# Kernel tuning notes

Hardware: AMD Instinct MI355X
Metric: run time of the kernel (lower is better)

## Reference

```python
import jax, jax.numpy as jnp
import numpy as np

BIG_K = 13
EPS = 1e-5  # torch BatchNorm2d default


def setup_inputs() -> dict:
    key = jax.random.key(0)
    k1, k2, k3, k4 = jax.random.split(key, 4)
    B, C1, C2, H, W_ = 8, 256, 256, 64, 64
    x = jax.random.normal(k1, (B, C1, H, W_), dtype=jnp.float32)
    # scale kernel by fan-in so pre-BN activations are O(1)
    fan_in = C1 * BIG_K * BIG_K
    W = jax.random.normal(k2, (C2, C1, BIG_K, BIG_K), dtype=jnp.float32) / np.sqrt(fan_in)
    gamma = jnp.ones((C2,), dtype=jnp.float32)
    beta = jnp.zeros((C2,), dtype=jnp.float32)
    running_mean = jax.random.normal(k3, (C2,), dtype=jnp.float32) * 0.1
    running_var = jax.random.uniform(k4, (C2,), dtype=jnp.float32, minval=0.5, maxval=1.5)
    return {"x": x, "W": W, "gamma": gamma, "beta": beta,
            "running_mean": running_mean, "running_var": running_var}


def reference(x, W, gamma, beta, running_mean, running_var):
    # Fallback path of ShiftWiseConv: big-kernel conv (no bias) -> BN (inference) -> SiLU
    pad = BIG_K // 2
    y = jax.lax.conv_general_dilated(
        x, W,
        window_strides=(1, 1),
        padding=[(pad, pad), (pad, pad)],
        dimension_numbers=("NCHW", "OIHW", "NCHW"),
    )
    inv = gamma * jax.lax.rsqrt(running_var + EPS)  # [C2]
    y = y * inv[None, :, None, None] + (beta - running_mean * inv)[None, :, None, None]
    return jax.nn.silu(y)
```

## Files before the change

### kernel.cpp

```cpp
#include <hip/hip_runtime.h>
#include <stdint.h>

#define EPS 1e-5f

typedef __attribute__((ext_vector_type(8))) __bf16 bf16x8;
typedef __attribute__((ext_vector_type(16))) float f32x16;

__device__ __forceinline__ int swz4(int r) { return (r ^ (r >> 2)) & 3; }

__device__ __forceinline__ unsigned short f2bf(float f) {
  union { float f; unsigned u; } v; v.f = f;
  unsigned r = v.u + 0x7fffu + ((v.u >> 16) & 1u);
  return (unsigned short)(r >> 16);
}

__device__ __forceinline__ void glds16(const unsigned short* g, unsigned short* l) {
  __builtin_amdgcn_global_load_lds(
      (const __attribute__((address_space(1))) void*)g,
      (__attribute__((address_space(3))) void*)l, 16, 0, 0);
}
__device__ __forceinline__ void glds4(const unsigned short* g, unsigned short* l) {
  __builtin_amdgcn_global_load_lds(
      (const __attribute__((address_space(1))) void*)g,
      (__attribute__((address_space(3))) void*)l, 4, 0, 0);
}

template <int N>
__device__ __forceinline__ void vmwait() {
  asm volatile("s_waitcnt vmcnt(%0)" ::"n"(N) : "memory");
}

__global__ __launch_bounds__(256) void pack_w_kernel(
    const float* __restrict__ W, unsigned short* __restrict__ Wp) {
  const int blk = blockIdx.x;
  const int c2 = blk / 13, kh = blk - c2 * 13;
  const int c1 = threadIdx.x;
  const int c2t = c2 >> 7, m = c2 & 127;
  const int c1c = c1 >> 5, c1i = c1 & 31;
  const float* src = W + (((size_t)(c2 * 256 + c1)) * 13 + kh) * 13;
  const int rowoff = (((c1i >> 3) ^ swz4(m)) << 3) + (c1i & 7);
#pragma unroll
  for (int kw = 0; kw < 13; ++kw) {
    const int ks = (kh * 8 + c1c) * 13 + kw;
    const size_t dst = (((size_t)c2t * 1352 + ks) * 128 + m) * 32 + rowoff;
    Wp[dst] = f2bf(src[kw]);
  }
}

__global__ __launch_bounds__(256) void pack_xt_kernel(
    const float* __restrict__ x, unsigned short* __restrict__ xT) {
  const int blk = blockIdx.x;
  const int rowp = blk % 76;
  const int bc = blk / 76;
  const int c1c = bc & 7, b = bc >> 3;
  const int row = rowp - 6;
  const bool rok = (unsigned)row < 64u;
  unsigned short* dst = xT + (size_t)blk * 2560;
  const float* srcb = x + (size_t)(b * 256 + c1c * 32) * 4096 +
                      (rok ? row * 64 : 0);
#pragma unroll
  for (int e = 0; e < 10; ++e) {
    const int idx = e * 256 + threadIdx.x;
    const int colp = idx >> 5, c1i = idx & 31;
    const int ic = colp - 8;
    const float v = (rok && (unsigned)ic < 64u) ? srcb[(size_t)c1i * 4096 + ic] : 0.f;
    dst[colp * 32 + ((((c1i >> 3) ^ swz4(colp)) << 3)) + (c1i & 7)] = f2bf(v);
  }
}

__global__ __launch_bounds__(256, 2) void conv5_kernel(
    const unsigned short* __restrict__ Wp, const unsigned short* __restrict__ xT,
    const float* __restrict__ gamma, const float* __restrict__ beta,
    const float* __restrict__ mean, const float* __restrict__ var,
    float* __restrict__ out) {
  __shared__ __align__(16) unsigned short Abuf[2][8192];
  __shared__ __align__(16) unsigned short Wbuf[2][5120];
  __shared__ float s_scale[128], s_shift[128];

  const int tid = threadIdx.x;
  const int bid = blockIdx.x;
  const int b = bid & 7;
  const int h0 = ((bid >> 3) & 31) * 2;
  const int c2t = bid >> 8;

  const int wid = tid >> 6, lane = tid & 63;
  const int wr = wid >> 1, wc = wid & 1;
  const int l31 = lane & 31, hi2 = lane >> 5;

  if (tid < 128) {
    const int c2 = c2t * 128 + tid;
    const float inv = gamma[c2] * rsqrtf(var[c2] + EPS);
    s_scale[tid] = inv;
    s_shift[tid] = beta[c2] - mean[c2] * inv;
  }

  int aoff[2][2];
#pragma unroll
  for (int mt = 0; mt < 2; ++mt)
#pragma unroll
    for (int ks = 0; ks < 2; ++ks) {
      const int m = wr * 64 + mt * 32 + l31;
      aoff[mt][ks] = m * 64 + (((ks * 2 + hi2) ^ swz4(m)) << 4);
    }
  int ndh[2], nwl[2];
#pragma unroll
  for (int nt = 0; nt < 2; ++nt) {
    const int n = wc * 64 + nt * 32 + l31;
    ndh[nt] = n >> 6;
    nwl[nt] = n & 63;
  }

  const int tid8 = tid * 8, tid2 = tid * 2;
  const int widA = wid * 512, wid128 = wid * 128;

  const size_t c2base = (size_t)c2t * 1352;
  const int bc8 = b * 8;

  auto wtile = [&](int T) -> const unsigned short* {
    const int kh = T >> 3, c1c = T & 7;
    return xT + (size_t)((bc8 + c1c) * 76 + h0 + kh) * 2560;
  };

  f32x16 acc[2][2];
#pragma unroll
  for (int i = 0; i < 2; ++i)
#pragma unroll
    for (int j = 0; j < 2; ++j)
#pragma unroll
      for (int r = 0; r < 16; ++r) acc[i][j][r] = 0.f;

  {
    const unsigned short* at0 = Wp + (c2base << 12);
    const unsigned short* at1 = Wp + ((c2base + 1) << 12);
    glds16(at0 + tid8, &Abuf[0][0] + widA);
    glds16(at0 + 2048 + tid8, &Abuf[0][2048] + widA);
    glds16(at1 + tid8, &Abuf[0][4096] + widA);
    glds16(at1 + 2048 + tid8, &Abuf[0][6144] + widA);
    const unsigned short* ws = wtile(0);
    glds16(ws + tid8, &Wbuf[0][0] + widA);
    glds16(ws + 2048 + tid8, &Wbuf[0][2048] + widA);
    glds4(ws + 4096 + tid2, &Wbuf[0][4096] + wid128);
    glds4(ws + 4608 + tid2, &Wbuf[0][4608] + wid128);
  }

#define CHALF(AB_, WB_, KW_)                                                  \
  {                                                                           \
    _Pragma("unroll") for (int ks = 0; ks < 2; ++ks) {                        \
      const bf16x8 a0 = *(const bf16x8*)((AB_) + aoff[0][ks]);                \
      const bf16x8 a1 = *(const bf16x8*)((AB_) + aoff[1][ks]);                \
      bf16x8 bfr[2];                                                          \
      _Pragma("unroll") for (int nt = 0; nt < 2; ++nt) {                      \
        const int wcoln = nwl[nt] + (KW_) + 2;                                \
        bfr[nt] = *(const bf16x8*)((WB_) + (ndh[nt] * 80 + wcoln) * 64 +      \
                                   (((ks * 2 + hi2) ^ swz4(wcoln)) << 4));    \
      }                                                                       \
      acc[0][0] = __builtin_amdgcn_mfma_f32_32x32x16_bf16(a0, bfr[0],         \
                                                          acc[0][0], 0, 0, 0);\
      acc[0][1] = __builtin_amdgcn_mfma_f32_32x32x16_bf16(a0, bfr[1],         \
                                                          acc[0][1], 0, 0, 0);\
      acc[1][0] = __builtin_amdgcn_mfma_f32_32x32x16_bf16(a1, bfr[0],         \
                                                          acc[1][0], 0, 0, 0);\
      acc[1][1] = __builtin_amdgcn_mfma_f32_32x32x16_bf16(a1, bfr[1],         \
                                                          acc[1][1], 0, 0, 0);\
    }                                                                         \
  }

#define PHASE(PH, KWA, WBA, KWB, WBB, WRT, WSRCP, WDB)                        \
  {                                                                           \
    {                                                                         \
      int sn0 = S0 + 2 * (PH) + 2;                                            \
      if (sn0 >= 1352) sn0 -= 1352;                                           \
      int sn1 = sn0 + 1;                                                      \
      if (sn1 >= 1352) sn1 -= 1352;                                           \
      const unsigned short* at0 = Wp + ((c2base + (size_t)sn0) << 12);        \
      const unsigned short* at1 = Wp + ((c2base + (size_t)sn1) << 12);        \
      unsigned short* ad = &Abuf[((PH) + 1) & 1][0];                          \
      glds16(at0 + tid8, ad + widA);                                          \
      glds16(at0 + 2048 + tid8, ad + 2048 + widA);                            \
      glds16(at1 + tid8, ad + 4096 + widA);                                   \
      glds16(at1 + 2048 + tid8, ad + 6144 + widA);                            \
    }                                                                         \
    if ((WRT) == 1) glds16((WSRCP) + tid8, &Wbuf[(WDB)][0] + widA);           \
    if ((WRT) == 2)                                                           \
      glds16((WSRCP) + 2048 + tid8, &Wbuf[(WDB)][2048] + widA);               \
    if ((WRT) == 3) {                                                         \
      glds4((WSRCP) + 4096 + tid2, &Wbuf[(WDB)][4096] + wid128);              \
      glds4((WSRCP) + 4608 + tid2, &Wbuf[(WDB)][4608] + wid128);              \
    }                                                                         \
    vmwait<((WRT) == 0 ? 4 : ((WRT) == 3 ? 6 : 5))>();                        \
    __builtin_amdgcn_s_barrier();                                             \
    asm volatile("" ::: "memory");                                            \
    {                                                                         \
      const char* abA = (const char*)&Abuf[(PH) & 1][0];                      \
      const char* abB = abA + 8192;                                           \
      const char* wbA = (const char*)&Wbuf[(WBA)][0];                         \
      const char* wbB = (const char*)&Wbuf[(WBB)][0];                         \
      __builtin_amdgcn_s_setprio(1);                                          \
      CHALF(abA, wbA, KWA)                                                    \
      CHALF(abB, wbB, KWB)                                                    \
      __builtin_amdgcn_s_setprio(0);                                          \
    }                                                                         \
    asm volatile("s_waitcnt lgkmcnt(0)" ::: "memory");                        \
    __builtin_amdgcn_s_barrier();                                             \
  }

  for (int u = 0; u < 26; ++u) {
    const int S0 = u * 52;
    const int Tb = u * 4;
    const unsigned short* wt1 = wtile(Tb + 1);
    const unsigned short* wt2 = wtile(Tb + 2);
    const unsigned short* wt3 = wtile(Tb + 3);
    const unsigned short* wt4 = wtile((Tb + 4 == 104) ? 0 : Tb + 4);
    PHASE(0, 0, 0, 1, 0, 0, wt1, 1)
    PHASE(1, 2, 0, 3, 0, 0, wt1, 1)
    PHASE(2, 4, 0, 5, 0, 0, wt1, 1)
    PHASE(3, 6, 0, 7, 0, 1, wt1, 1)
    PHASE(4, 8, 0, 9, 0, 2, wt1, 1)
    PHASE(5, 10, 0, 11, 0, 3, wt1, 1)
    PHASE(6, 12, 0, 0, 1, 0, wt1, 1)
    PHASE(7, 1, 1, 2, 1, 0, wt2, 0)
    PHASE(8, 3, 1, 4, 1, 0, wt2, 0)
    PHASE(9, 5, 1, 6, 1, 1, wt2, 0)
    PHASE(10, 7, 1, 8, 1, 2, wt2, 0)
    PHASE(11, 9, 1, 10, 1, 3, wt2, 0)
    PHASE(12, 11, 1, 12, 1, 0, wt2, 0)
    PHASE(13, 0, 0, 1, 0, 0, wt3, 1)
    PHASE(14, 2, 0, 3, 0, 0, wt3, 1)
    PHASE(15, 4, 0, 5, 0, 0, wt3, 1)
    PHASE(16, 6, 0, 7, 0, 1, wt3, 1)
    PHASE(17, 8, 0, 9, 0, 2, wt3, 1)
    PHASE(18, 10, 0, 11, 0, 3, wt3, 1)
    PHASE(19, 12, 0, 0, 1, 0, wt3, 1)
    PHASE(20, 1, 1, 2, 1, 0, wt4, 0)
    PHASE(21, 3, 1, 4, 1, 0, wt4, 0)
    PHASE(22, 5, 1, 6, 1, 1, wt4, 0)
    PHASE(23, 7, 1, 8, 1, 2, wt4, 0)
    PHASE(24, 9, 1, 10, 1, 3, wt4, 0)
    PHASE(25, 11, 1, 12, 1, 0, wt4, 0)
  }
#undef PHASE
#undef CHALF

  vmwait<0>();

#pragma unroll
  for (int mt = 0; mt < 2; ++mt) {
#pragma unroll
    for (int nt = 0; nt < 2; ++nt) {
      const int n = wc * 64 + nt * 32 + l31;
      const int hh = h0 + (n >> 6), ww = n & 63;
#pragma unroll
      for (int r = 0; r < 16; ++r) {
        const int mloc = (r & 3) + 8 * (r >> 2) + 4 * hi2;
        const int c2l = wr * 64 + mt * 32 + mloc;
        const float y = acc[mt][nt][r] * s_scale[c2l] + s_shift[c2l];
        out[((size_t)(b * 256 + c2t * 128 + c2l)) * 4096 + hh * 64 + ww] =
            y / (1.f + __expf(-y));
      }
    }
  }
}

__global__ void naive_conv_kernel(
    const float* __restrict__ x, const float* __restrict__ W,
    const float* __restrict__ gamma, const float* __restrict__ beta,
    const float* __restrict__ mean, const float* __restrict__ var,
    float* __restrict__ out) {
  const int idx = blockIdx.x * 256 + threadIdx.x;
  if (idx >= 8 * 256 * 64 * 64) return;
  const int w = idx & 63, h = (idx >> 6) & 63;
  const int c2 = (idx >> 12) & 255, b = idx >> 20;
  float s = 0.f;
  for (int c1 = 0; c1 < 256; ++c1) {
    const float* xp = x + ((size_t)(b * 256 + c1) * 4096);
    const float* wp = W + ((size_t)(c2 * 256 + c1) * 169);
    for (int kh = 0; kh < 13; ++kh) {
      const int r = h + kh - 6;
      if ((unsigned)r >= 64u) continue;
      for (int kw = 0; kw < 13; ++kw) {
        const int c = w + kw - 6;
        if ((unsigned)c >= 64u) continue;
        s += xp[r * 64 + c] * wp[kh * 13 + kw];
      }
    }
  }
  const float inv = gamma[c2] * rsqrtf(var[c2] + EPS);
  const float y = s * inv + (beta[c2] - mean[c2] * inv);
  out[idx] = y / (1.f + __expf(-y));
}

extern "C" void kernel_launch(void* const* d_in, const int* in_sizes, int n_in,
                              void* d_out, int out_size, void* d_ws, size_t ws_size,
                              hipStream_t stream) {
  const float* x = (const float*)d_in[0];
  const float* W = (const float*)d_in[1];
  const float* gamma = (const float*)d_in[2];
  const float* beta = (const float*)d_in[3];
  const float* mean = (const float*)d_in[4];
  const float* var = (const float*)d_in[5];
  float* out = (float*)d_out;

  const size_t WP_BYTES = (size_t)256 * 43264 * 2;
  const size_t XT_BYTES = (size_t)12455424 * 2;

  if (ws_size >= WP_BYTES + XT_BYTES) {
    unsigned short* Wp = (unsigned short*)d_ws;
    unsigned short* xT = (unsigned short*)((char*)d_ws + WP_BYTES);
    pack_w_kernel<<<256 * 13, 256, 0, stream>>>(W, Wp);
    pack_xt_kernel<<<8 * 8 * 76, 256, 0, stream>>>(x, xT);
    conv5_kernel<<<512, 256, 0, stream>>>(Wp, xT, gamma, beta, mean, var, out);
  } else {
    naive_conv_kernel<<<(8 * 256 * 64 * 64 + 255) / 256, 256, 0, stream>>>(
        x, W, gamma, beta, mean, var, out);
  }
}
```

Measured before the change: 641.6 us.

## Prefetch LDS fragments to registers and defer global-load wait past MFMAs

Each phase now reads all A and W fragments for both half-steps from LDS into registers first. It then issues the next tile's global-to-LDS loads, passes a barrier, and runs 16 back-to-back MFMAs. The vmcnt wait for the prefetched tiles moves to the end of the phase, after the MFMAs, so the global loads overlap compute instead of stalling before it. The cost is about 64 more VGPRs per thread for the staged fragments, which may pressure occupancy under the 2-block launch bound or cause spills.

Result: faster. 624.0 us (-2.7%).

```diff
diff --git a/kernel.cpp b/kernel.cpp
--- a/kernel.cpp
+++ b/kernel.cpp
@@ -68,7 +68,7 @@
   }
 }
 
-__global__ __launch_bounds__(256, 2) void conv5_kernel(
+__global__ __launch_bounds__(256, 2) void conv6_kernel(
     const unsigned short* __restrict__ Wp, const unsigned short* __restrict__ xT,
     const float* __restrict__ gamma, const float* __restrict__ beta,
     const float* __restrict__ mean, const float* __restrict__ var,
@@ -128,6 +128,8 @@
     for (int j = 0; j < 2; ++j)
 #pragma unroll
       for (int r = 0; r < 16; ++r) acc[i][j][r] = 0.f;
+
+  bf16x8 rA[2][2][2], rB[2][2][2];
 
   {
     const unsigned short* at0 = Wp + (c2base << 12);
@@ -141,32 +143,36 @@
     glds16(ws + 2048 + tid8, &Wbuf[0][2048] + widA);
     glds4(ws + 4096 + tid2, &Wbuf[0][4096] + wid128);
     glds4(ws + 4608 + tid2, &Wbuf[0][4608] + wid128);
-  }
-
-#define CHALF(AB_, WB_, KW_)                                                  \
-  {                                                                           \
-    _Pragma("unroll") for (int ks = 0; ks < 2; ++ks) {                        \
-      const bf16x8 a0 = *(const bf16x8*)((AB_) + aoff[0][ks]);                \
-      const bf16x8 a1 = *(const bf16x8*)((AB_) + aoff[1][ks]);                \
-      bf16x8 bfr[2];                                                          \
-      _Pragma("unroll") for (int nt = 0; nt < 2; ++nt) {                      \
-        const int wcoln = nwl[nt] + (KW_) + 2;                                \
-        bfr[nt] = *(const bf16x8*)((WB_) + (ndh[nt] * 80 + wcoln) * 64 +      \
-                                   (((ks * 2 + hi2) ^ swz4(wcoln)) << 4));    \
-      }                                                                       \
-      acc[0][0] = __builtin_amdgcn_mfma_f32_32x32x16_bf16(a0, bfr[0],         \
-                                                          acc[0][0], 0, 0, 0);\
-      acc[0][1] = __builtin_amdgcn_mfma_f32_32x32x16_bf16(a0, bfr[1],         \
-                                                          acc[0][1], 0, 0, 0);\
-      acc[1][0] = __builtin_amdgcn_mfma_f32_32x32x16_bf16(a1, bfr[0],         \
-                                                          acc[1][0], 0, 0, 0);\
-      acc[1][1] = __builtin_amdgcn_mfma_f32_32x32x16_bf16(a1, bfr[1],         \
-                                                          acc[1][1], 0, 0, 0);\
-    }                                                                         \
+    vmwait<0>();
+    __builtin_amdgcn_s_barrier();
   }
 
 #define PHASE(PH, KWA, WBA, KWB, WBB, WRT, WSRCP, WDB)                        \
   {                                                                           \
+      \
+    {                                                                         \
+      const char* abA = (const char*)&Abuf[(PH) & 1][0];                      \
+      const char* abB = abA + 8192;                                           \
+      const char* wbA = (const char*)&Wbuf[(WBA)][0];                         \
+      const char* wbB = (const char*)&Wbuf[(WBB)][0];                         \
+      _Pragma("unroll") for (int ks = 0; ks < 2; ++ks) {                      \
+        rA[0][ks][0] = *(const bf16x8*)(abA + aoff[0][ks]);                   \
+        rA[0][ks][1] = *(const bf16x8*)(abA + aoff[1][ks]);                   \
+        rA[1][ks][0] = *(const bf16x8*)(abB + aoff[0][ks]);                   \
+        rA[1][ks][1] = *(const bf16x8*)(abB + aoff[1][ks]);                   \
+        _Pragma("unroll") for (int nt = 0; nt < 2; ++nt) {                    \
+          const int colA = nwl[nt] + (KWA) + 2;                               \
+          rB[0][ks][nt] = *(const bf16x8*)(                                   \
+              wbA + (ndh[nt] * 80 + colA) * 64 +                              \
+              (((ks * 2 + hi2) ^ swz4(colA)) << 4));                          \
+          const int colB = nwl[nt] + (KWB) + 2;                               \
+          rB[1][ks][nt] = *(const bf16x8*)(                                   \
+              wbB + (ndh[nt] * 80 + colB) * 64 +                              \
+              (((ks * 2 + hi2) ^ swz4(colB)) << 4));                          \
+        }                                                                     \
+      }                                                                       \
+    }                                                                         \
+                   \
     {                                                                         \
       int sn0 = S0 + 2 * (PH) + 2;                                            \
       if (sn0 >= 1352) sn0 -= 1352;                                           \
@@ -187,20 +193,27 @@
       glds4((WSRCP) + 4096 + tid2, &Wbuf[(WDB)][4096] + wid128);              \
       glds4((WSRCP) + 4608 + tid2, &Wbuf[(WDB)][4608] + wid128);              \
     }                                                                         \
-    vmwait<((WRT) == 0 ? 4 : ((WRT) == 3 ? 6 : 5))>();                        \
+    asm volatile("" ::: "memory");       \
     __builtin_amdgcn_s_barrier();                                             \
-    asm volatile("" ::: "memory");                                            \
+    __builtin_amdgcn_sched_barrier(0);              \
+           \
     {                                                                         \
-      const char* abA = (const char*)&Abuf[(PH) & 1][0];                      \
-      const char* abB = abA + 8192;                                           \
-      const char* wbA = (const char*)&Wbuf[(WBA)][0];                         \
-      const char* wbB = (const char*)&Wbuf[(WBB)][0];                         \
       __builtin_amdgcn_s_setprio(1);                                          \
-      CHALF(abA, wbA, KWA)                                                    \
-      CHALF(abB, wbB, KWB)                                                    \
+      _Pragma("unroll") for (int s = 0; s < 2; ++s)                           \
+          _Pragma("unroll") for (int ks = 0; ks < 2; ++ks) {                  \
+        acc[0][0] = __builtin_amdgcn_mfma_f32_32x32x16_bf16(                  \
+            rA[s][ks][0], rB[s][ks][0], acc[0][0], 0, 0, 0);                  \
+        acc[0][1] = __builtin_amdgcn_mfma_f32_32x32x16_bf16(                  \
+            rA[s][ks][0], rB[s][ks][1], acc[0][1], 0, 0, 0);                  \
+        acc[1][0] = __builtin_amdgcn_mfma_f32_32x32x16_bf16(                  \
+            rA[s][ks][1], rB[s][ks][0], acc[1][0], 0, 0, 0);                  \
+        acc[1][1] = __builtin_amdgcn_mfma_f32_32x32x16_bf16(                  \
+            rA[s][ks][1], rB[s][ks][1], acc[1][1], 0, 0, 0);                  \
+      }                                                                       \
       __builtin_amdgcn_s_setprio(0);                                          \
     }                                                                         \
-    asm volatile("s_waitcnt lgkmcnt(0)" ::: "memory");                        \
+            \
+    vmwait<((WRT) == 0 ? 0 : ((WRT) == 3 ? 2 : 1))>();                        \
     __builtin_amdgcn_s_barrier();                                             \
   }
 
@@ -239,7 +252,6 @@
     PHASE(25, 11, 1, 12, 1, 0, wt4, 0)
   }
 #undef PHASE
-#undef CHALF
 
   vmwait<0>();
 
@@ -308,7 +320,7 @@
     unsigned short* xT = (unsigned short*)((char*)d_ws + WP_BYTES);
     pack_w_kernel<<<256 * 13, 256, 0, stream>>>(W, Wp);
     pack_xt_kernel<<<8 * 8 * 76, 256, 0, stream>>>(x, xT);
-    conv5_kernel<<<512, 256, 0, stream>>>(Wp, xT, gamma, beta, mean, var, out);
+    conv6_kernel<<<512, 256, 0, stream>>>(Wp, xT, gamma, beta, mean, var, out);
   } else {
     naive_conv_kernel<<<(8 * 256 * 64 * 64 + 255) / 256, 256, 0, stream>>>(
         x, W, gamma, beta, mean, var, out);
```

## Restructure conv main loop into four-phase pipeline with larger A staging buffer

Applied to the files above, without the earlier changes.

Replaces the 26-phase double-buffered loop, which issued one A-tile pair per barrier, with a 104-iteration loop. Each iteration has four phases that stage 3-4 weight slices into a 7-slot (28672-element) LDS ring and explicitly prefetch fragments into registers ahead of the MFMAs. The W-tile for the next kh/c1 step is swapped via pointers. This cuts the barrier count per unit of MFMA work and interleaves LDS reads with MFMAs. In exchange it uses more LDS and registers, which may hurt the two-blocks-per-CU occupancy, and it waits for all outstanding loads (vmcnt 0) every phase, so less global latency is hidden.

New measurement: 639.9 us. Within noise of the previous version (-0.3%).

```diff
diff --git a/kernel.cpp b/kernel.cpp
--- a/kernel.cpp
+++ b/kernel.cpp
@@ -68,12 +68,12 @@
   }
 }
 
-__global__ __launch_bounds__(256, 2) void conv5_kernel(
+__global__ __launch_bounds__(256, 2) void conv12_kernel(
     const unsigned short* __restrict__ Wp, const unsigned short* __restrict__ xT,
     const float* __restrict__ gamma, const float* __restrict__ beta,
     const float* __restrict__ mean, const float* __restrict__ var,
     float* __restrict__ out) {
-  __shared__ __align__(16) unsigned short Abuf[2][8192];
+  __shared__ __align__(16) unsigned short Abuf[28672];
   __shared__ __align__(16) unsigned short Wbuf[2][5120];
   __shared__ float s_scale[128], s_shift[128];
 
@@ -94,13 +94,13 @@
     s_shift[tid] = beta[c2] - mean[c2] * inv;
   }
 
-  int aoff[2][2];
+  int aoffs[2][2];
 #pragma unroll
   for (int mt = 0; mt < 2; ++mt)
 #pragma unroll
     for (int ks = 0; ks < 2; ++ks) {
       const int m = wr * 64 + mt * 32 + l31;
-      aoff[mt][ks] = m * 64 + (((ks * 2 + hi2) ^ swz4(m)) << 4);
+      aoffs[mt][ks] = m * 64 + (((ks * 2 + hi2) ^ swz4(m)) << 4);
     }
   int ndh[2], nwl[2];
 #pragma unroll
@@ -115,6 +115,8 @@
 
   const size_t c2base = (size_t)c2t * 1352;
   const int bc8 = b * 8;
+  const char* Abase = (const char*)&Abuf[0];
+  unsigned short* AbaseU = &Abuf[0];
 
   auto wtile = [&](int T) -> const unsigned short* {
     const int kh = T >> 3, c1c = T & 7;
@@ -129,119 +131,135 @@
 #pragma unroll
       for (int r = 0; r < 16; ++r) acc[i][j][r] = 0.f;
 
+  bf16x8 fA0[2][2], fB0[2][2], fA1[2][2], fB1[2][2];
+  bf16x8 fA2[2][2], fB2[2][2], fA3[2][2], fB3[2][2];
+
+  unsigned short* wcurU = &Wbuf[0][0];
+  unsigned short* wnxtU = &Wbuf[1][0];
+  const char* wbC = (const char*)wcurU;
+
   {
-    const unsigned short* at0 = Wp + (c2base << 12);
-    const unsigned short* at1 = Wp + ((c2base + 1) << 12);
-    glds16(at0 + tid8, &Abuf[0][0] + widA);
-    glds16(at0 + 2048 + tid8, &Abuf[0][2048] + widA);
-    glds16(at1 + tid8, &Abuf[0][4096] + widA);
-    glds16(at1 + 2048 + tid8, &Abuf[0][6144] + widA);
     const unsigned short* ws = wtile(0);
-    glds16(ws + tid8, &Wbuf[0][0] + widA);
-    glds16(ws + 2048 + tid8, &Wbuf[0][2048] + widA);
-    glds4(ws + 4096 + tid2, &Wbuf[0][4096] + wid128);
-    glds4(ws + 4608 + tid2, &Wbuf[0][4608] + wid128);
-  }
-
-#define CHALF(AB_, WB_, KW_)                                                  \
+    glds16(ws + tid8, wcurU + widA);
+    glds16(ws + 2048 + tid8, wcurU + 2048 + widA);
+    glds4(ws + 4096 + tid2, wcurU + 4096 + wid128);
+    glds4(ws + 4608 + tid2, wcurU + 4608 + wid128);
+#pragma unroll
+    for (int i = 0; i < 3; ++i) {
+      const unsigned short* at = Wp + ((c2base + (size_t)i) << 12);
+      glds16(at + tid8, AbaseU + i * 4096 + widA);
+      glds16(at + 2048 + tid8, AbaseU + i * 4096 + 2048 + widA);
+    }
+    vmwait<0>();
+    __builtin_amdgcn_s_barrier();
+    __builtin_amdgcn_sched_barrier(0);
+  }
+
+#define READF(FA, FB, ABOFF, KW)                                              \
   {                                                                           \
+    const char* ab_ = Abase + 2 * (ABOFF);                                    \
     _Pragma("unroll") for (int ks = 0; ks < 2; ++ks) {                        \
-      const bf16x8 a0 = *(const bf16x8*)((AB_) + aoff[0][ks]);                \
-      const bf16x8 a1 = *(const bf16x8*)((AB_) + aoff[1][ks]);                \
-      bf16x8 bfr[2];                                                          \
+      FA[ks][0] = *(const bf16x8*)(ab_ + aoffs[0][ks]);                       \
+      FA[ks][1] = *(const bf16x8*)(ab_ + aoffs[1][ks]);                       \
       _Pragma("unroll") for (int nt = 0; nt < 2; ++nt) {                      \
-        const int wcoln = nwl[nt] + (KW_) + 2;                                \
-        bfr[nt] = *(const bf16x8*)((WB_) + (ndh[nt] * 80 + wcoln) * 64 +      \
-                                   (((ks * 2 + hi2) ^ swz4(wcoln)) << 4));    \
+        const int c_ = nwl[nt] + (KW) + 2;                                    \
+        FB[ks][nt] = *(const bf16x8*)(wbC + (ndh[nt] * 80 + c_) * 64 +        \
+                                      (((ks * 2 + hi2) ^ swz4(c_)) << 4));    \
       }                                                                       \
-      acc[0][0] = __builtin_amdgcn_mfma_f32_32x32x16_bf16(a0, bfr[0],         \
-                                                          acc[0][0], 0, 0, 0);\
-      acc[0][1] = __builtin_amdgcn_mfma_f32_32x32x16_bf16(a0, bfr[1],         \
-                                                          acc[0][1], 0, 0, 0);\
-      acc[1][0] = __builtin_amdgcn_mfma_f32_32x32x16_bf16(a1, bfr[0],         \
-                                                          acc[1][0], 0, 0, 0);\
-      acc[1][1] = __builtin_amdgcn_mfma_f32_32x32x16_bf16(a1, bfr[1],         \
-                                                          acc[1][1], 0, 0, 0);\
     }                                                                         \
   }
 
-#define PHASE(PH, KWA, WBA, KWB, WBB, WRT, WSRCP, WDB)                        \
-  {                                                                           \
-    {                                                                         \
-      int sn0 = S0 + 2 * (PH) + 2;                                            \
-      if (sn0 >= 1352) sn0 -= 1352;                                           \
-      int sn1 = sn0 + 1;                                                      \
-      if (sn1 >= 1352) sn1 -= 1352;                                           \
-      const unsigned short* at0 = Wp + ((c2base + (size_t)sn0) << 12);        \
-      const unsigned short* at1 = Wp + ((c2base + (size_t)sn1) << 12);        \
-      unsigned short* ad = &Abuf[((PH) + 1) & 1][0];                          \
-      glds16(at0 + tid8, ad + widA);                                          \
-      glds16(at0 + 2048 + tid8, ad + 2048 + widA);                            \
-      glds16(at1 + tid8, ad + 4096 + widA);                                   \
-      glds16(at1 + 2048 + tid8, ad + 6144 + widA);                            \
-    }                                                                         \
-    if ((WRT) == 1) glds16((WSRCP) + tid8, &Wbuf[(WDB)][0] + widA);           \
-    if ((WRT) == 2)                                                           \
-      glds16((WSRCP) + 2048 + tid8, &Wbuf[(WDB)][2048] + widA);               \
-    if ((WRT) == 3) {                                                         \
-      glds4((WSRCP) + 4096 + tid2, &Wbuf[(WDB)][4096] + wid128);              \
-      glds4((WSRCP) + 4608 + tid2, &Wbuf[(WDB)][4608] + wid128);              \
-    }                                                                         \
-    vmwait<((WRT) == 0 ? 4 : ((WRT) == 3 ? 6 : 5))>();                        \
-    __builtin_amdgcn_s_barrier();                                             \
-    asm volatile("" ::: "memory");                                            \
-    {                                                                         \
-      const char* abA = (const char*)&Abuf[(PH) & 1][0];                      \
-      const char* abB = abA + 8192;                                           \
-      const char* wbA = (const char*)&Wbuf[(WBA)][0];                         \
-      const char* wbB = (const char*)&Wbuf[(WBB)][0];                         \
-      __builtin_amdgcn_s_setprio(1);                                          \
-      CHALF(abA, wbA, KWA)                                                    \
-      CHALF(abB, wbB, KWB)                                                    \
-      __builtin_amdgcn_s_setprio(0);                                          \
-    }                                                                         \
-    asm volatile("s_waitcnt lgkmcnt(0)" ::: "memory");                        \
-    __builtin_amdgcn_s_barrier();                                             \
-  }
-
-  for (int u = 0; u < 26; ++u) {
-    const int S0 = u * 52;
-    const int Tb = u * 4;
-    const unsigned short* wt1 = wtile(Tb + 1);
-    const unsigned short* wt2 = wtile(Tb + 2);
-    const unsigned short* wt3 = wtile(Tb + 3);
-    const unsigned short* wt4 = wtile((Tb + 4 == 104) ? 0 : Tb + 4);
-    PHASE(0, 0, 0, 1, 0, 0, wt1, 1)
-    PHASE(1, 2, 0, 3, 0, 0, wt1, 1)
-    PHASE(2, 4, 0, 5, 0, 0, wt1, 1)
-    PHASE(3, 6, 0, 7, 0, 1, wt1, 1)
-    PHASE(4, 8, 0, 9, 0, 2, wt1, 1)
-    PHASE(5, 10, 0, 11, 0, 3, wt1, 1)
-    PHASE(6, 12, 0, 0, 1, 0, wt1, 1)
-    PHASE(7, 1, 1, 2, 1, 0, wt2, 0)
-    PHASE(8, 3, 1, 4, 1, 0, wt2, 0)
-    PHASE(9, 5, 1, 6, 1, 1, wt2, 0)
-    PHASE(10, 7, 1, 8, 1, 2, wt2, 0)
-    PHASE(11, 9, 1, 10, 1, 3, wt2, 0)
-    PHASE(12, 11, 1, 12, 1, 0, wt2, 0)
-    PHASE(13, 0, 0, 1, 0, 0, wt3, 1)
-    PHASE(14, 2, 0, 3, 0, 0, wt3, 1)
-    PHASE(15, 4, 0, 5, 0, 0, wt3, 1)
-    PHASE(16, 6, 0, 7, 0, 1, wt3, 1)
-    PHASE(17, 8, 0, 9, 0, 2, wt3, 1)
-    PHASE(18, 10, 0, 11, 0, 3, wt3, 1)
-    PHASE(19, 12, 0, 0, 1, 0, wt3, 1)
-    PHASE(20, 1, 1, 2, 1, 0, wt4, 0)
-    PHASE(21, 3, 1, 4, 1, 0, wt4, 0)
-    PHASE(22, 5, 1, 6, 1, 1, wt4, 0)
-    PHASE(23, 7, 1, 8, 1, 2, wt4, 0)
-    PHASE(24, 9, 1, 10, 1, 3, wt4, 0)
-    PHASE(25, 11, 1, 12, 1, 0, wt4, 0)
-  }
-#undef PHASE
-#undef CHALF
-
-  vmwait<0>();
+#define MF(FA, FB)                                                            \
+  _Pragma("unroll") for (int ks = 0; ks < 2; ++ks) {                          \
+    acc[0][0] = __builtin_amdgcn_mfma_f32_32x32x16_bf16(FA[ks][0], FB[ks][0], \
+                                                        acc[0][0], 0, 0, 0);  \
+    acc[0][1] = __builtin_amdgcn_mfma_f32_32x32x16_bf16(FA[ks][0], FB[ks][1], \
+                                                        acc[0][1], 0, 0, 0);  \
+    acc[1][0] = __builtin_amdgcn_mfma_f32_32x32x16_bf16(FA[ks][1], FB[ks][0], \
+                                                        acc[1][0], 0, 0, 0);  \
+    acc[1][1] = __builtin_amdgcn_mfma_f32_32x32x16_bf16(FA[ks][1], FB[ks][1], \
+                                                        acc[1][1], 0, 0, 0);  \
+  }
+
+#define PREA(NN, KS0, NABASE)                                                 \
+  _Pragma("unroll") for (int i = 0; i < (NN); ++i) {                          \
+    const unsigned short* at =                                                \
+        Wp + ((c2base + (size_t)((KS0) + i)) << 12);                          \
+    unsigned short* ad = AbaseU + (NABASE) + i * 4096;                        \
+    glds16(at + tid8, ad + widA);                                             \
+    glds16(at + 2048 + tid8, ad + 2048 + widA);                               \
+  }
+
+#define ENDPH                                                                 \
+  vmwait<0>();                                                                \
+  __builtin_amdgcn_s_barrier();                                               \
+  __builtin_amdgcn_sched_barrier(0);
+
+  for (int t = 0; t < 104; ++t) {
+    const int t13 = t * 13;
+    const int tn = (t == 103) ? 0 : t + 1;
+    const int tn13 = tn * 13;
+    const unsigned short* wsrc = wtile(tn);
+
+    PREA(4, t13 + 3, 12288)
+    glds16(wsrc + tid8, wnxtU + widA);
+    READF(fA0, fB0, 0, 0)
+    __builtin_amdgcn_s_setprio(1);
+    READF(fA1, fB1, 4096, 1)
+    MF(fA0, fB0)
+    READF(fA2, fB2, 8192, 2)
+    MF(fA1, fB1)
+    MF(fA2, fB2)
+    __builtin_amdgcn_s_setprio(0);
+    ENDPH
+
+    PREA(3, t13 + 7, 0)
+    glds16(wsrc + 2048 + tid8, wnxtU + 2048 + widA);
+    READF(fA0, fB0, 12288, 3)
+    __builtin_amdgcn_s_setprio(1);
+    READF(fA1, fB1, 16384, 4)
+    MF(fA0, fB0)
+    READF(fA2, fB2, 20480, 5)
+    MF(fA1, fB1)
+    READF(fA3, fB3, 24576, 6)
+    MF(fA2, fB2)
+    MF(fA3, fB3)
+    __builtin_amdgcn_s_setprio(0);
+    ENDPH
+
+    PREA(3, t13 + 10, 12288)
+    glds4(wsrc + 4096 + tid2, wnxtU + 4096 + wid128);
+    glds4(wsrc + 4608 + tid2, wnxtU + 4608 + wid128);
+    READF(fA0, fB0, 0, 7)
+    __builtin_amdgcn_s_setprio(1);
+    READF(fA1, fB1, 4096, 8)
+    MF(fA0, fB0)
+    READF(fA2, fB2, 8192, 9)
+    MF(fA1, fB1)
+    MF(fA2, fB2)
+    __builtin_amdgcn_s_setprio(0);
+    ENDPH
+
+    PREA(3, tn13, 0)
+    READF(fA0, fB0, 12288, 10)
+    __builtin_amdgcn_s_setprio(1);
+    READF(fA1, fB1, 16384, 11)
+    MF(fA0, fB0)
+    READF(fA2, fB2, 20480, 12)
+    MF(fA1, fB1)
+    MF(fA2, fB2)
+    __builtin_amdgcn_s_setprio(0);
+    ENDPH
+
+    unsigned short* tw = wcurU;
+    wcurU = wnxtU;
+    wnxtU = tw;
+    wbC = (const char*)wcurU;
+  }
+#undef READF
+#undef MF
+#undef PREA
+#undef ENDPH
 
 #pragma unroll
   for (int mt = 0; mt < 2; ++mt) {
@@ -308,7 +326,7 @@
     unsigned short* xT = (unsigned short*)((char*)d_ws + WP_BYTES);
     pack_w_kernel<<<256 * 13, 256, 0, stream>>>(W, Wp);
     pack_xt_kernel<<<8 * 8 * 76, 256, 0, stream>>>(x, xT);
-    conv5_kernel<<<512, 256, 0, stream>>>(Wp, xT, gamma, beta, mean, var, out);
+    conv12_kernel<<<512, 256, 0, stream>>>(Wp, xT, gamma, beta, mean, var, out);
   } else {
     naive_conv_kernel<<<(8 * 256 * 64 * 64 + 255) / 256, 256, 0, stream>>>(
         x, W, gamma, beta, mean, var, out);
```
